# Optimization experiments

Hardware: AMD Instinct MI355X
Metric: run time of the kernel (lower is better)

The kernel has to match this reference:

```python
import jax, jax.numpy as jnp
import numpy as np

N_GENE = 50000
N_PROT = 50000
E = 500000
D = 128          # embedding_dim
C = 32           # out_channels = embedding_dim // attn_heads
F_IN = 256       # in_channels per node type
NUM_MP = 3       # metapaths: [gene-gene, gene-protein, protein-protein]


def _glorot(key, shape):
    lim = float(np.sqrt(6.0 / (shape[0] + shape[1])))
    return jax.random.uniform(key, shape, minval=-lim, maxval=lim, dtype=jnp.float32)


def setup_inputs() -> dict:
    key = jax.random.key(0)
    ks = jax.random.split(key, 24)
    inp = {
        "x_gene": jax.random.normal(ks[0], (N_GENE, F_IN), dtype=jnp.float32),
        "x_protein": jax.random.normal(ks[1], (N_PROT, F_IN), dtype=jnp.float32),
        # node-type projections linear_l / linear_r
        "Wl_gene": _glorot(ks[2], (D, F_IN)), "bl_gene": jnp.zeros((D,), jnp.float32),
        "Wr_gene": _glorot(ks[3], (D, F_IN)), "br_gene": jnp.zeros((D,), jnp.float32),
        "Wl_prot": _glorot(ks[4], (D, F_IN)), "bl_prot": jnp.zeros((D,), jnp.float32),
        "Wr_prot": _glorot(ks[5], (D, F_IN)), "br_prot": jnp.zeros((D,), jnp.float32),
        # per-metapath attention params (stacked over 3 metapaths)
        "alW": jnp.stack([_glorot(ks[6 + i], (C, D)) for i in range(NUM_MP)]),
        "alb": jnp.zeros((NUM_MP, C), jnp.float32),
        "arW": jnp.stack([_glorot(ks[9 + i], (C, D)) for i in range(NUM_MP)]),
        "arb": jnp.zeros((NUM_MP, C), jnp.float32),
        "qw": jnp.stack([_glorot(ks[12 + i], (2 * C, 1)) for i in range(NUM_MP)]),
        "sharp": jnp.ones((NUM_MP,), jnp.float32),  # 'sharpening' alpha_activation
        # per-node-type relation-weighting conv (Linear(D, 1))
        "conv_gene_W": _glorot(ks[15], (1, D)), "conv_gene_b": jnp.zeros((1,), jnp.float32),
        "conv_prot_W": _glorot(ks[16], (1, D)), "conv_prot_b": jnp.zeros((1,), jnp.float32),
        # edge indices: row 0 = head node (aggregation target), row 1 = tail node
        "edge_gg": jax.random.randint(ks[17], (2, E), 0, N_GENE, dtype=jnp.int32),
        "edge_gp": jnp.stack([jax.random.randint(ks[18], (E,), 0, N_GENE, dtype=jnp.int32),
                               jax.random.randint(ks[19], (E,), 0, N_PROT, dtype=jnp.int32)]),
        "edge_pp": jax.random.randint(ks[20], (2, E), 0, N_PROT, dtype=jnp.int32),
    }
    return inp


def _segment_softmax(scores, seg, n):
    # numerically stable softmax over variable-size neighborhoods (grouped by seg)
    m = jax.ops.segment_max(scores, seg, num_segments=n)
    m = jnp.where(jnp.isfinite(m), m, 0.0)
    ex = jnp.exp(scores - m[seg])
    denom = jax.ops.segment_sum(ex, seg, num_segments=n)
    return ex / (denom[seg] + 1e-16)


def _metapath_agg(l_head, r_tail, alW, alb, arW, arb, qw, sharp, eidx, n_head):
    # alpha_l / alpha_r node-level projections [N, C]
    al = l_head @ alW.T + alb
    ar = r_tail @ arW.T + arb
    src, dst = eidx[0], eidx[1]           # head (aggregate-at), tail (message-from)
    a_i = al[src]                          # [E, C]
    a_j = ar[dst]                          # [E, C]
    # attn_q: Tanh then Linear(2C -> 1, no bias); 'sharpening' scales the logit
    e = (jnp.tanh(jnp.concatenate([a_i, a_j], axis=1)) @ qw)[:, 0] * sharp  # [E]
    alpha = _segment_softmax(e, src, n_head)
    # message x_j * alpha, scatter-add into head nodes (aggr='add')
    return jax.ops.segment_sum(r_tail[dst] * alpha[:, None], src, num_segments=n_head)


def _relation_combine(aggs, l_self, conv_W, conv_b):
    # stack relation embeddings + self embedding: [N, R, D]
    out = jnp.stack(aggs + [l_self], axis=1)
    beta = jax.nn.softmax(out @ conv_W.T + conv_b, axis=1)  # [N, R, 1]
    return jax.nn.relu(jnp.sum(out * beta, axis=1))          # [N, D]


def reference(x_gene, x_protein, Wl_gene, bl_gene, Wr_gene, br_gene,
              Wl_prot, bl_prot, Wr_prot, br_prot,
              alW, alb, arW, arb, qw, sharp,
              conv_gene_W, conv_gene_b, conv_prot_W, conv_prot_b,
              edge_gg, edge_gp, edge_pp):
    # first layer: l/r projections from raw features
    l_gene = x_gene @ Wl_gene.T + bl_gene
    r_gene = x_gene @ Wr_gene.T + br_gene
    l_prot = x_protein @ Wl_prot.T + bl_prot
    r_prot = x_protein @ Wr_prot.T + br_prot

    # metapath 0: gene <- gene ; metapath 1: gene <- protein ; metapath 2: protein <- protein
    agg_gg = _metapath_agg(l_gene, r_gene, alW[0], alb[0], arW[0], arb[0], qw[0], sharp[0], edge_gg, N_GENE)
    agg_gp = _metapath_agg(l_gene, r_prot, alW[1], alb[1], arW[1], arb[1], qw[1], sharp[1], edge_gp, N_GENE)
    agg_pp = _metapath_agg(l_prot, r_prot, alW[2], alb[2], arW[2], arb[2], qw[2], sharp[2], edge_pp, N_PROT)

    out_gene = _relation_combine([agg_gg, agg_gp], l_gene, conv_gene_W, conv_gene_b)
    out_prot = _relation_combine([agg_pp], l_prot, conv_prot_W, conv_prot_b)
    return (out_gene, out_prot)
```

## Files before the change

### kernel.cpp

```cpp
#include <hip/hip_runtime.h>
#include <hip/hip_bf16.h>


typedef __attribute__((ext_vector_type(8))) short short8;
typedef __attribute__((ext_vector_type(4))) float floatx4;

__device__ __forceinline__ void gload16(const void* g, void* l) {
  __builtin_amdgcn_global_load_lds(
      (const __attribute__((address_space(1))) void*)g,
      (__attribute__((address_space(3))) void*)l, 16, 0, 0);
}

__device__ __forceinline__ ushort f2b(float x) {
  __hip_bfloat16 h = __float2bfloat16(x);
  return *reinterpret_cast<ushort*>(&h);
}
__device__ __forceinline__ float b2f_lo(unsigned v) { return __uint_as_float(v << 16); }
__device__ __forceinline__ float b2f_hi(unsigned v) { return __uint_as_float(v & 0xffff0000u); }

struct CvtArgs {
  const float* src[8];
  ushort* dst[8];
  int valid[8];
  int total[8];
  int bstart[9];
};
__global__ __launch_bounds__(256) void cvt_multi(CvtArgs a) {
  int b = blockIdx.x;
  int e = 0;
#pragma unroll
  for (int j = 1; j < 8; ++j)
    if (b >= a.bstart[j]) e = j;
  int i = ((b - a.bstart[e]) * 256 + threadIdx.x) * 4;
  if (i >= a.total[e]) return;
  float4 v = make_float4(0.f, 0.f, 0.f, 0.f);
  if (i < a.valid[e]) v = *(const float4*)(a.src[e] + i);
  ushort4 o;
  o.x = f2b(v.x); o.y = f2b(v.y); o.z = f2b(v.z); o.w = f2b(v.w);
  *(ushort4*)(a.dst[e] + i) = o;
}

struct ProjArgs {
  const float* x[2];
  const ushort* Wb[2];
  const float* bl[2];
  const float* br[2];
  ushort* lb[2];
  ushort* rb[2];
  int N[2];
  const ushort* aW[4];
  const float* ab[4];
  const float* q0[4];
  const float* q1[4];
  float* o0[4];
  float* o1[4];
  int BN[4];
};
__global__ __launch_bounds__(256) void proj_lr_mfma(ProjArgs g) {
  const int ty = blockIdx.z;
  const float* xp = g.x[ty];
  const int N = g.N[ty];
  __shared__ float Asf[2 * 128 * 32];
  __shared__ ushort Bs[2 * 128 * 32];
  const int tid = threadIdx.x;
  const int lane = tid & 63;
  const int wv = tid >> 6;
  const int wm = wv & 1, wn = wv >> 1;
  const int rowBase = blockIdx.x * 128;
  const int colHalf = blockIdx.y;
  const ushort* Wbase = g.Wb[ty] + (size_t)colHalf * 128 * 256;

  floatx4 acc[4][4] = {};

  auto stage = [&](int buf, int k0) {
#pragma unroll
    for (int i = 0; i < 4; ++i) {
      const int G = i * 256 + wv * 64 + lane;
      const int row = G >> 3;
      const int cg = (G & 7) ^ (row & 7);
      const int xr = min(rowBase + row, N - 1);
      gload16(xp + (size_t)xr * 256 + k0 + cg * 4, &Asf[buf * 4096 + G * 4]);
    }
#pragma unroll
    for (int i = 0; i < 2; ++i) {
      const int G = i * 256 + wv * 64 + lane;
      const int row = G >> 2;
      const int cg = (G & 3) ^ ((row >> 1) & 3);
      gload16(Wbase + (size_t)row * 256 + k0 + cg * 8, &Bs[buf * 4096 + G * 8]);
    }
  };

  stage(0, 0);
  __syncthreads();

  int t = 0;
  for (int k0 = 0; k0 < 256; k0 += 32) {
    if (k0 < 224) stage(t ^ 1, k0 + 32);
    const float* Ab = &Asf[t * 4096];
    const ushort* Bb = &Bs[t * 4096];
    short8 bf[4];
#pragma unroll
    for (int nt = 0; nt < 4; ++nt) {
      const int row = wn * 64 + nt * 16 + (lane & 15);
      const int c = (lane >> 4) ^ ((row >> 1) & 3);
      bf[nt] = *(const short8*)&Bb[(row * 4 + c) * 8];
    }
#pragma unroll
    for (int mt = 0; mt < 4; ++mt) {
      const int row = wm * 64 + mt * 16 + (lane & 15);
      const int c0 = ((lane >> 4) * 2) ^ (row & 7);
      const int c1 = ((lane >> 4) * 2 + 1) ^ (row & 7);
      float4 f0 = *(const float4*)&Ab[(row * 8 + c0) * 4];
      float4 f1 = *(const float4*)&Ab[(row * 8 + c1) * 4];
      short8 a;
      a[0] = (short)f2b(f0.x); a[1] = (short)f2b(f0.y);
      a[2] = (short)f2b(f0.z); a[3] = (short)f2b(f0.w);
      a[4] = (short)f2b(f1.x); a[5] = (short)f2b(f1.y);
      a[6] = (short)f2b(f1.z); a[7] = (short)f2b(f1.w);
#pragma unroll
      for (int nt = 0; nt < 4; ++nt)
        acc[mt][nt] = __builtin_amdgcn_mfma_f32_16x16x32_bf16(a, bf[nt], acc[mt][nt], 0, 0, 0);
    }
    __syncthreads();
    t ^= 1;
  }

  ushort* tile = (ushort*)Asf;
  const float* bias = colHalf ? g.br[ty] : g.bl[ty];
  ushort* outp = colHalf ? g.rb[ty] : g.lb[ty];
#pragma unroll
  for (int mt = 0; mt < 4; ++mt)
#pragma unroll
    for (int nt = 0; nt < 4; ++nt) {
      int col = wn * 64 + nt * 16 + (lane & 15);
      float bv = bias[col];
#pragma unroll
      for (int vi = 0; vi < 4; ++vi) {
        int row = wm * 64 + mt * 16 + (lane >> 4) * 4 + vi;
        ushort v = f2b(acc[mt][nt][vi] + bv);
        tile[row * 128 + (((col >> 3) ^ (row & 15)) << 3) + (col & 7)] = v;
        if (rowBase + row < N) outp[(size_t)(rowBase + row) * 128 + col] = v;
      }
    }
  __syncthreads();

  const int e = ty * 2 + colHalf;
  const int NB = g.BN[e] >> 4;
  const ushort* aW = g.aW[e];
  floatx4 acc2[2][4] = {};
  for (int k0 = 0; k0 < 128; k0 += 32) {
    short8 bf2[4];
#pragma unroll
    for (int nt = 0; nt < 4; ++nt)
      if (nt < NB)
        bf2[nt] = *(const short8*)(aW + (size_t)(nt * 16 + (lane & 15)) * 128 +
                                   k0 + (lane >> 4) * 8);
#pragma unroll
    for (int mt = 0; mt < 2; ++mt) {
      const int row = wv * 32 + mt * 16 + (lane & 15);
      const int c8 = (k0 >> 3) + (lane >> 4);
      short8 a = *(const short8*)&tile[row * 128 + ((c8 ^ (row & 15)) << 3)];
#pragma unroll
      for (int nt = 0; nt < 4; ++nt)
        if (nt < NB)
          acc2[mt][nt] = __builtin_amdgcn_mfma_f32_16x16x32_bf16(a, bf2[nt], acc2[mt][nt], 0, 0, 0);
    }
  }

  const float* ab = g.ab[e];
  const int l15 = lane & 15;
  const bool two = (NB == 4);
  float bv2[4];
#pragma unroll
  for (int nt = 0; nt < 4; ++nt) bv2[nt] = (nt < NB) ? ab[nt * 16 + l15] : 0.f;
  float q0v0 = g.q0[e][l15], q0v1 = g.q0[e][16 + l15];
  float q1v0 = 0.f, q1v1 = 0.f;
  if (two) { q1v0 = g.q1[e][l15]; q1v1 = g.q1[e][16 + l15]; }
  float* o0 = g.o0[e];
  float* o1 = g.o1[e];
#pragma unroll
  for (int mt = 0; mt < 2; ++mt)
#pragma unroll
    for (int vi = 0; vi < 4; ++vi) {
      float slo = tanhf(acc2[mt][0][vi] + bv2[0]) * q0v0
                + tanhf(acc2[mt][1][vi] + bv2[1]) * q0v1;
      float shi = 0.f;
      if (two)
        shi = tanhf(acc2[mt][2][vi] + bv2[2]) * q1v0
            + tanhf(acc2[mt][3][vi] + bv2[3]) * q1v1;
#pragma unroll
      for (int m = 8; m >= 1; m >>= 1) {
        slo += __shfl_xor(slo, m, 64);
        shi += __shfl_xor(shi, m, 64);
      }
      const int row = rowBase + wv * 32 + mt * 16 + (lane >> 4) * 4 + vi;
      if (l15 == 0 && row < N) {
        o0[row] = slo;
        if (two) o1[row] = shi;
      }
    }
}

__global__ __launch_bounds__(256) void hist3_kernel(
    const int* __restrict__ e0, const int* __restrict__ e1,
    const int* __restrict__ e2, int* __restrict__ deg,
    int* __restrict__ rank, int E, int NG) {
  int e = blockIdx.x * 256 + threadIdx.x;
  if (e >= 3 * E) return;
  int mp = (e >= 2 * E) ? 2 : ((e >= E) ? 1 : 0);
  int el = e - mp * E;
  const int* ep = (mp == 0) ? e0 : (mp == 1) ? e1 : e2;
  int segb = (mp == 2) ? 2 * NG : mp * NG;
  rank[e] = atomicAdd(&deg[segb + ep[el]], 1);
}

__global__ __launch_bounds__(256) void scanA_kernel(
    const int* __restrict__ deg, int* __restrict__ offsets,
    int* __restrict__ tile_tot, int n) {
  __shared__ int wtot[4];
  const int t = threadIdx.x;
  const int base = blockIdx.x * 2048 + t * 8;
  int v[8], pre[8], s = 0;
#pragma unroll
  for (int j = 0; j < 8; ++j) {
    v[j] = (base + j < n) ? deg[base + j] : 0;
    pre[j] = s;
    s += v[j];
  }
  const int lane = t & 63, wv = t >> 6;
  int x = s;
#pragma unroll
  for (int o = 1; o < 64; o <<= 1) {
    int u = __shfl_up(x, o, 64);
    if (lane >= o) x += u;
  }
  if (lane == 63) wtot[wv] = x;
  __syncthreads();
  int wpre = 0;
#pragma unroll
  for (int j = 0; j < 4; ++j) wpre += (j < wv) ? wtot[j] : 0;
  int excl = wpre + x - s;
#pragma unroll
  for (int j = 0; j < 8; ++j)
    if (base + j < n) offsets[base + j] = excl + pre[j];
  if (t == 255) tile_tot[blockIdx.x] = wpre + x;
}

__global__ __launch_bounds__(256) void scanB_kernel(
    const int* __restrict__ tile_tot, int* __restrict__ tile_pre,
    int* __restrict__ offsets, int T, int n) {
  __shared__ int wtot[4];
  const int t = threadIdx.x;
  int v = (t < T) ? tile_tot[t] : 0;
  const int lane = t & 63, wv = t >> 6;
  int x = v;
#pragma unroll
  for (int o = 1; o < 64; o <<= 1) {
    int u = __shfl_up(x, o, 64);
    if (lane >= o) x += u;
  }
  if (lane == 63) wtot[wv] = x;
  __syncthreads();
  int wpre = 0;
#pragma unroll
  for (int j = 0; j < 4; ++j) wpre += (j < wv) ? wtot[j] : 0;
  if (t < T) tile_pre[t] = wpre + x - v;
  if (t == 255) offsets[n] = wpre + x;
}

__global__ __launch_bounds__(256) void scanC_kernel(
    int* __restrict__ offsets, const int* __restrict__ tile_pre, int n) {
  const int add = tile_pre[blockIdx.x];
  const int base = blockIdx.x * 2048 + threadIdx.x * 8;
#pragma unroll
  for (int j = 0; j < 8; ++j)
    if (base + j < n) offsets[base + j] += add;
}

__global__ __launch_bounds__(256) void scatter3_kernel(
    const int* __restrict__ e0, const int* __restrict__ e1,
    const int* __restrict__ e2, const int* __restrict__ rank,
    const int* __restrict__ offsets,
    const float* __restrict__ tl3, const float* __restrict__ tr3,
    const float* __restrict__ sharp, int2* __restrict__ recs,
    int E, int NG, int NP) {
  int e = blockIdx.x * 256 + threadIdx.x;
  if (e >= 3 * E) return;
  int mp = (e >= 2 * E) ? 2 : ((e >= E) ? 1 : 0);
  int el = e - mp * E;
  const int* ep = (mp == 0) ? e0 : (mp == 1) ? e1 : e2;
  int s = ep[el], d = ep[el + E];
  int hb = (mp == 2) ? 2 * NG : mp * NG;
  int tb = (mp == 0) ? 0 : (mp == 1) ? NG : NG + NP;
  float w = expf((tl3[hb + s] + tr3[tb + d]) * sharp[mp]);
  recs[offsets[hb + s] + rank[e]] = make_int2(d << 8, __float_as_int(w));
}

__global__ __launch_bounds__(256) void gather_combine(
    const ushort* __restrict__ rb_gene, const ushort* __restrict__ rb_prot,
    const ushort* __restrict__ lb_gene, const ushort* __restrict__ lb_prot,
    const int* __restrict__ offsets, const int2* __restrict__ recs,
    const float* __restrict__ cgW, const float* __restrict__ cgb,
    const float* __restrict__ cpW, const float* __restrict__ cpb,
    float* __restrict__ out_gene, float* __restrict__ out_prot,
    int NG, int NP) {
  const int lane = threadIdx.x & 63;
  const int l16 = lane & 15;
  const int node = blockIdx.x * 16 + (threadIdx.x >> 4);
  if (node >= NG + NP) return;
  const bool isGene = node < NG;
  const unsigned coloff = (unsigned)l16 << 4;
  const unsigned OMASK = 0x00FFFF00u;

  const int h0 = isGene ? node : NG + node;
  const int j0a = offsets[h0];
  const int ca = offsets[h0 + 1] - j0a;
  int j0b = 0, cb2 = 0;
  if (isGene) {
    j0b = offsets[NG + node];
    cb2 = offsets[NG + node + 1] - j0b;
  }

  float a0[8] = {0.f, 0.f, 0.f, 0.f, 0.f, 0.f, 0.f, 0.f};
  float a1[8] = {0.f, 0.f, 0.f, 0.f, 0.f, 0.f, 0.f, 0.f};
  float ds0 = 0.f, ds1 = 0.f;
  const ushort* rtA = isGene ? rb_gene : rb_prot;

  if (isGene) {
    const int cmax = (ca > cb2) ? ca : cb2;
    if (cmax > 0) {
      int2 rA[4], rB[4];
#pragma unroll
      for (int p = 0; p < 4; ++p) {
        rA[p] = recs[j0a + ((p < ca) ? p : 0)];
        rB[p] = recs[j0b + ((p < cb2) ? p : 0)];
      }
      const int nit = (cmax + 3) >> 2;
      for (int it = 0; it < nit; ++it) {
        const int b = it * 4;
        float wA[4], wB[4];
        uint4 vA[4], vB[4];
#pragma unroll
        for (int p = 0; p < 4; ++p) {
          wA[p] = (b + p < ca)  ? __int_as_float(rA[p].y) : 0.f;
          wB[p] = (b + p < cb2) ? __int_as_float(rB[p].y) : 0.f;
          vA[p] = *(const uint4*)((const char*)rtA + (((unsigned)rA[p].x & OMASK) + coloff));
          vB[p] = *(const uint4*)((const char*)rb_prot + (((unsigned)rB[p].x & OMASK) + coloff));
        }
        const int nb = b + 4;
#pragma unroll
        for (int p = 0; p < 4; ++p) {
          rA[p] = recs[j0a + ((nb + p < ca) ? nb + p : 0)];
          rB[p] = recs[j0b + ((nb + p < cb2) ? nb + p : 0)];
        }
#pragma unroll
        for (int p = 0; p < 4; ++p) {
          ds0 += wA[p];
          a0[0] += b2f_lo(vA[p].x) * wA[p]; a0[1] += b2f_hi(vA[p].x) * wA[p];
          a0[2] += b2f_lo(vA[p].y) * wA[p]; a0[3] += b2f_hi(vA[p].y) * wA[p];
          a0[4] += b2f_lo(vA[p].z) * wA[p]; a0[5] += b2f_hi(vA[p].z) * wA[p];
          a0[6] += b2f_lo(vA[p].w) * wA[p]; a0[7] += b2f_hi(vA[p].w) * wA[p];
          ds1 += wB[p];
          a1[0] += b2f_lo(vB[p].x) * wB[p]; a1[1] += b2f_hi(vB[p].x) * wB[p];
          a1[2] += b2f_lo(vB[p].y) * wB[p]; a1[3] += b2f_hi(vB[p].y) * wB[p];
          a1[4] += b2f_lo(vB[p].z) * wB[p]; a1[5] += b2f_hi(vB[p].z) * wB[p];
          a1[6] += b2f_lo(vB[p].w) * wB[p]; a1[7] += b2f_hi(vB[p].w) * wB[p];
        }
      }
    }
  } else {
    if (ca > 0) {
      int2 r0 = recs[j0a];
      int2 r1 = recs[j0a + ((1 < ca) ? 1 : 0)];
      int2 r2 = recs[j0a + ((2 < ca) ? 2 : 0)];
      int2 r3 = recs[j0a + ((3 < ca) ? 3 : 0)];
      const int nit = (ca + 3) >> 2;
      for (int it = 0; it < nit; ++it) {
        const int b = it * 4;
        const float w0 = (b < ca)     ? __int_as_float(r0.y) : 0.f;
        const float w1 = (b + 1 < ca) ? __int_as_float(r1.y) : 0.f;
        const float w2 = (b + 2 < ca) ? __int_as_float(r2.y) : 0.f;
        const float w3 = (b + 3 < ca) ? __int_as_float(r3.y) : 0.f;
        const uint4 v0 = *(const uint4*)((const char*)rtA + (((unsigned)r0.x & OMASK) + coloff));
        const uint4 v1 = *(const uint4*)((const char*)rtA + (((unsigned)r1.x & OMASK) + coloff));
        const uint4 v2 = *(const uint4*)((const char*)rtA + (((unsigned)r2.x & OMASK) + coloff));
        const uint4 v3 = *(const uint4*)((const char*)rtA + (((unsigned)r3.x & OMASK) + coloff));
        const int nb = b + 4;
        r0 = recs[j0a + ((nb < ca) ? nb : 0)];
        r1 = recs[j0a + ((nb + 1 < ca) ? nb + 1 : 0)];
        r2 = recs[j0a + ((nb + 2 < ca) ? nb + 2 : 0)];
        r3 = recs[j0a + ((nb + 3 < ca) ? nb + 3 : 0)];
        ds0 += (w0 + w1) + (w2 + w3);
        a0[0] += b2f_lo(v0.x) * w0 + b2f_lo(v1.x) * w1 + b2f_lo(v2.x) * w2 + b2f_lo(v3.x) * w3;
        a0[1] += b2f_hi(v0.x) * w0 + b2f_hi(v1.x) * w1 + b2f_hi(v2.x) * w2 + b2f_hi(v3.x) * w3;
        a0[2] += b2f_lo(v0.y) * w0 + b2f_lo(v1.y) * w1 + b2f_lo(v2.y) * w2 + b2f_lo(v3.y) * w3;
        a0[3] += b2f_hi(v0.y) * w0 + b2f_hi(v1.y) * w1 + b2f_hi(v2.y) * w2 + b2f_hi(v3.y) * w3;
        a0[4] += b2f_lo(v0.z) * w0 + b2f_lo(v1.z) * w1 + b2f_lo(v2.z) * w2 + b2f_lo(v3.z) * w3;
        a0[5] += b2f_hi(v0.z) * w0 + b2f_hi(v1.z) * w1 + b2f_hi(v2.z) * w2 + b2f_hi(v3.z) * w3;
        a0[6] += b2f_lo(v0.w) * w0 + b2f_lo(v1.w) * w1 + b2f_lo(v2.w) * w2 + b2f_lo(v3.w) * w3;
        a0[7] += b2f_hi(v0.w) * w0 + b2f_hi(v1.w) * w1 + b2f_hi(v2.w) * w2 + b2f_hi(v3.w) * w3;
      }
    }
  }

  const float inv0 = 1.f / (ds0 + 1e-16f);
  const float inv1 = 1.f / (ds1 + 1e-16f);
  float g0[8], g1[8], self[8];
#pragma unroll
  for (int c = 0; c < 8; ++c) { g0[c] = a0[c] * inv0; g1[c] = a1[c] * inv1; }
  {
    const ushort* lbp = isGene ? lb_gene + (size_t)node * 128
                               : lb_prot + (size_t)(node - NG) * 128;
    uint4 sv = *(const uint4*)(lbp + l16 * 8);
    self[0] = b2f_lo(sv.x); self[1] = b2f_hi(sv.x);
    self[2] = b2f_lo(sv.y); self[3] = b2f_hi(sv.y);
    self[4] = b2f_lo(sv.z); self[5] = b2f_hi(sv.z);
    self[6] = b2f_lo(sv.w); self[7] = b2f_hi(sv.w);
  }

  const float* cW = isGene ? cgW : cpW;
  const float cb = isGene ? cgb[0] : cpb[0];
  const float4 wlo = *(const float4*)(cW + l16 * 8);
  const float4 whi = *(const float4*)(cW + l16 * 8 + 4);
  float p0 = g0[0] * wlo.x + g0[1] * wlo.y + g0[2] * wlo.z + g0[3] * wlo.w +
             g0[4] * whi.x + g0[5] * whi.y + g0[6] * whi.z + g0[7] * whi.w;
  float p1 = g1[0] * wlo.x + g1[1] * wlo.y + g1[2] * wlo.z + g1[3] * wlo.w +
             g1[4] * whi.x + g1[5] * whi.y + g1[6] * whi.z + g1[7] * whi.w;
  float ps = self[0] * wlo.x + self[1] * wlo.y + self[2] * wlo.z + self[3] * wlo.w +
             self[4] * whi.x + self[5] * whi.y + self[6] * whi.z + self[7] * whi.w;
#pragma unroll
  for (int m = 8; m >= 1; m >>= 1) {
    p0 += __shfl_xor(p0, m, 64);
    p1 += __shfl_xor(p1, m, 64);
    ps += __shfl_xor(ps, m, 64);
  }
  const float s0 = p0 + cb, s1 = p1 + cb, ss = ps + cb;
  const float mx = isGene ? fmaxf(fmaxf(s0, s1), ss) : fmaxf(s0, ss);
  const float e0 = expf(s0 - mx);
  const float e1 = isGene ? expf(s1 - mx) : 0.f;
  const float es = expf(ss - mx);
  const float sum = e0 + e1 + es;
  const float b0 = e0 / sum, b1 = e1 / sum, bs = es / sum;

  float4 o0, o1;
  o0.x = fmaxf(g0[0] * b0 + g1[0] * b1 + self[0] * bs, 0.f);
  o0.y = fmaxf(g0[1] * b0 + g1[1] * b1 + self[1] * bs, 0.f);
  o0.z = fmaxf(g0[2] * b0 + g1[2] * b1 + self[2] * bs, 0.f);
  o0.w = fmaxf(g0[3] * b0 + g1[3] * b1 + self[3] * bs, 0.f);
  o1.x = fmaxf(g0[4] * b0 + g1[4] * b1 + self[4] * bs, 0.f);
  o1.y = fmaxf(g0[5] * b0 + g1[5] * b1 + self[5] * bs, 0.f);
  o1.z = fmaxf(g0[6] * b0 + g1[6] * b1 + self[6] * bs, 0.f);
  o1.w = fmaxf(g0[7] * b0 + g1[7] * b1 + self[7] * bs, 0.f);
  float* op = isGene ? out_gene + (size_t)node * 128
                     : out_prot + (size_t)(node - NG) * 128;
  *(float4*)(op + l16 * 8) = o0;
  *(float4*)(op + l16 * 8 + 4) = o1;
}

extern "C" void kernel_launch(void* const* d_in, const int* in_sizes, int n_in,
                              void* d_out, int out_size, void* d_ws,
                              size_t ws_size, hipStream_t stream) {
  const float* x_gene  = (const float*)d_in[0];
  const float* x_prot  = (const float*)d_in[1];
  const float* Wl_gene = (const float*)d_in[2];
  const float* bl_gene = (const float*)d_in[3];
  const float* Wr_gene = (const float*)d_in[4];
  const float* br_gene = (const float*)d_in[5];
  const float* Wl_prot = (const float*)d_in[6];
  const float* bl_prot = (const float*)d_in[7];
  const float* Wr_prot = (const float*)d_in[8];
  const float* br_prot = (const float*)d_in[9];
  const float* alW     = (const float*)d_in[10];
  const float* alb     = (const float*)d_in[11];
  const float* arW     = (const float*)d_in[12];
  const float* arb     = (const float*)d_in[13];
  const float* qw      = (const float*)d_in[14];
  const float* sharp   = (const float*)d_in[15];
  const float* cgW     = (const float*)d_in[16];
  const float* cgb     = (const float*)d_in[17];
  const float* cpW     = (const float*)d_in[18];
  const float* cpb     = (const float*)d_in[19];
  const int* e_gg      = (const int*)d_in[20];
  const int* e_gp      = (const int*)d_in[21];
  const int* e_pp      = (const int*)d_in[22];

  const int NG = in_sizes[0] / 256;
  const int NP = in_sizes[1] / 256;
  const int E  = in_sizes[20] / 2;
  const int NPG = (NG + 127) & ~127;
  const int NT = 2 * NG + NP;
  const int NR = NG + 2 * NP;

  char* base = (char*)d_ws;
  size_t off = 0;
  auto alloc = [&](size_t bytes) {
    void* p = base + off;
    off = (off + bytes + 255) & ~(size_t)255;
    return p;
  };
  ushort* Wlr_gene = (ushort*)alloc(256 * 256 * 2);
  ushort* Wlr_prot = (ushort*)alloc(256 * 256 * 2);
  ushort* alWb     = (ushort*)alloc(96 * 128 * 2);
  ushort* arWb     = (ushort*)alloc(96 * 128 * 2);
  ushort* lb_gene  = (ushort*)alloc((size_t)NPG * 128 * 2);
  ushort* rb_gene  = (ushort*)alloc((size_t)NPG * 128 * 2);
  ushort* lb_prot  = (ushort*)alloc((size_t)NPG * 128 * 2);
  ushort* rb_prot  = (ushort*)alloc((size_t)NPG * 128 * 2);
  int*    deg      = (int*)alloc((size_t)NT * 4);
  int*    offsets  = (int*)alloc((size_t)(NT + 1) * 4);
  const int TILES  = (NT + 2047) / 2048;
  int*    tile_tot = (int*)alloc((size_t)TILES * 4);
  int*    tile_pre = (int*)alloc((size_t)TILES * 4);
  int*    rank     = (int*)alloc((size_t)(3 * E) * 4);
  int2*   recs     = (int2*)alloc((size_t)(3 * E) * sizeof(int2));
  float*  tl3      = (float*)alloc((size_t)NT * 4);
  float*  tr3      = (float*)alloc((size_t)NR * 4);

  float* out_gene = (float*)d_out;
  float* out_prot = out_gene + (size_t)NG * 128;

  dim3 blk(256);

  {
    CvtArgs a;
    const float* srcs[8] = {Wl_gene, Wr_gene, Wl_prot, Wr_prot, alW, arW,
                            Wl_gene, Wl_gene};
    ushort* dsts[8] = {Wlr_gene, Wlr_gene + 128 * 256,
                       Wlr_prot, Wlr_prot + 128 * 256, alWb, arWb,
                       Wlr_gene, Wlr_gene};
    int sizes[8] = {128 * 256, 128 * 256, 128 * 256, 128 * 256,
                    96 * 128, 96 * 128, 0, 0};
    int b = 0;
    for (int j = 0; j < 8; ++j) {
      a.src[j] = srcs[j]; a.dst[j] = dsts[j];
      a.valid[j] = sizes[j]; a.total[j] = sizes[j];
      a.bstart[j] = b;
      b += (sizes[j] / 4 + 255) / 256;
    }
    a.bstart[8] = b;
    cvt_multi<<<b, blk, 0, stream>>>(a);
  }

  {
    ProjArgs p;
    p.x[0] = x_gene; p.x[1] = x_prot;
    p.Wb[0] = Wlr_gene; p.Wb[1] = Wlr_prot;
    p.bl[0] = bl_gene; p.bl[1] = bl_prot;
    p.br[0] = br_gene; p.br[1] = br_prot;
    p.lb[0] = lb_gene; p.lb[1] = lb_prot;
    p.rb[0] = rb_gene; p.rb[1] = rb_prot;
    p.N[0] = NG; p.N[1] = NP;
    p.aW[0] = alWb;            p.ab[0] = alb;      p.BN[0] = 64;
    p.q0[0] = qw + 0;  p.q1[0] = qw + 64;  p.o0[0] = tl3;          p.o1[0] = tl3 + NG;
    p.aW[1] = arWb;            p.ab[1] = arb;      p.BN[1] = 32;
    p.q0[1] = qw + 32; p.q1[1] = qw + 32;  p.o0[1] = tr3;          p.o1[1] = tr3;
    p.aW[2] = alWb + 64 * 128; p.ab[2] = alb + 64; p.BN[2] = 32;
    p.q0[2] = qw + 128; p.q1[2] = qw + 128; p.o0[2] = tl3 + 2 * NG; p.o1[2] = tl3 + 2 * NG;
    p.aW[3] = arWb + 32 * 128; p.ab[3] = arb + 32; p.BN[3] = 64;
    p.q0[3] = qw + 96; p.q1[3] = qw + 160; p.o0[3] = tr3 + NG;     p.o1[3] = tr3 + NG + NP;
    proj_lr_mfma<<<dim3(NPG / 128, 2, 2), blk, 0, stream>>>(p);
  }

  const int gridE3 = (3 * E + 255) / 256;
  hipMemsetAsync(deg, 0, (size_t)NT * sizeof(int), stream);
  hist3_kernel<<<gridE3, blk, 0, stream>>>(e_gg, e_gp, e_pp, deg, rank, E, NG);
  scanA_kernel<<<TILES, blk, 0, stream>>>(deg, offsets, tile_tot, NT);
  scanB_kernel<<<1, blk, 0, stream>>>(tile_tot, tile_pre, offsets, TILES, NT);
  scanC_kernel<<<TILES, blk, 0, stream>>>(offsets, tile_pre, NT);
  scatter3_kernel<<<gridE3, blk, 0, stream>>>(e_gg, e_gp, e_pp, rank, offsets,
                                              tl3, tr3, sharp, recs, E, NG, NP);

  gather_combine<<<(NG + NP + 15) / 16, blk, 0, stream>>>(
      rb_gene, rb_prot, lb_gene, lb_prot, offsets, recs,
      cgW, cgb, cpW, cpb, out_gene, out_prot, NG, NP);
}
```

Measured before the change: 398.1 us.

## Fuse edge histogram into projection kernel launch as extra blocks

Merges the edge-degree histogram (atomic counting with rank capture) into the projection GEMM kernel by appending extra blocks that do the histogram work. The grid is flattened to 1D, with block index decoding for type, column half and row tile. This removes one kernel launch and lets the memory-bound atomic work overlap with the compute-bound MFMA projection. The cost is that the histogram blocks now carry the GEMM kernel's large shared-memory allocation, which may limit how many of them can be resident at once.

```diff
diff --git a/kernel.cpp b/kernel.cpp
--- a/kernel.cpp
+++ b/kernel.cpp
@@ -55,19 +55,42 @@
   float* o0[4];
   float* o1[4];
   int BN[4];
+  const int* e0;
+  const int* e1;
+  const int* e2;
+  int* deg;
+  int* rank;
+  int E;
+  int NGh;
+  int projBlocks;
 };
 __global__ __launch_bounds__(256) void proj_lr_mfma(ProjArgs g) {
-  const int ty = blockIdx.z;
-  const float* xp = g.x[ty];
-  const int N = g.N[ty];
   __shared__ float Asf[2 * 128 * 32];
   __shared__ ushort Bs[2 * 128 * 32];
   const int tid = threadIdx.x;
+
+  if ((int)blockIdx.x >= g.projBlocks) {
+    const int E = g.E;
+    int e = ((int)blockIdx.x - g.projBlocks) * 256 + tid;
+    if (e < 3 * E) {
+      int mp = (e >= 2 * E) ? 2 : ((e >= E) ? 1 : 0);
+      int el = e - mp * E;
+      const int* ep = (mp == 0) ? g.e0 : (mp == 1) ? g.e1 : g.e2;
+      int segb = (mp == 2) ? 2 * g.NGh : mp * g.NGh;
+      g.rank[e] = atomicAdd(&g.deg[segb + ep[el]], 1);
+    }
+    return;
+  }
+
+  const int pb = blockIdx.x;
+  const int ty = pb & 1;
+  const int colHalf = (pb >> 1) & 1;
+  const float* xp = g.x[ty];
+  const int N = g.N[ty];
   const int lane = tid & 63;
   const int wv = tid >> 6;
   const int wm = wv & 1, wn = wv >> 1;
-  const int rowBase = blockIdx.x * 128;
-  const int colHalf = blockIdx.y;
+  const int rowBase = (pb >> 2) * 128;
   const ushort* Wbase = g.Wb[ty] + (size_t)colHalf * 128 * 256;
 
   floatx4 acc[4][4] = {};
@@ -199,19 +222,6 @@
         if (two) o1[row] = shi;
       }
     }
-}
-
-__global__ __launch_bounds__(256) void hist3_kernel(
-    const int* __restrict__ e0, const int* __restrict__ e1,
-    const int* __restrict__ e2, int* __restrict__ deg,
-    int* __restrict__ rank, int E, int NG) {
-  int e = blockIdx.x * 256 + threadIdx.x;
-  if (e >= 3 * E) return;
-  int mp = (e >= 2 * E) ? 2 : ((e >= E) ? 1 : 0);
-  int el = e - mp * E;
-  const int* ep = (mp == 0) ? e0 : (mp == 1) ? e1 : e2;
-  int segb = (mp == 2) ? 2 * NG : mp * NG;
-  rank[e] = atomicAdd(&deg[segb + ep[el]], 1);
 }
 
 __global__ __launch_bounds__(256) void scanA_kernel(
@@ -521,6 +531,7 @@
 
   dim3 blk(256);
 
+  hipMemsetAsync(deg, 0, (size_t)NT * sizeof(int), stream);
   {
     CvtArgs a;
     const float* srcs[8] = {Wl_gene, Wr_gene, Wl_prot, Wr_prot, alW, arW,
@@ -541,6 +552,8 @@
     cvt_multi<<<b, blk, 0, stream>>>(a);
   }
 
+  const int gridE3 = (3 * E + 255) / 256;
+  const int projBlocks = (NPG / 128) * 4;
   {
     ProjArgs p;
     p.x[0] = x_gene; p.x[1] = x_prot;
@@ -558,12 +571,12 @@
     p.q0[2] = qw + 128; p.q1[2] = qw + 128; p.o0[2] = tl3 + 2 * NG; p.o1[2] = tl3 + 2 * NG;
     p.aW[3] = arWb + 32 * 128; p.ab[3] = arb + 32; p.BN[3] = 64;
     p.q0[3] = qw + 96; p.q1[3] = qw + 160; p.o0[3] = tr3 + NG;     p.o1[3] = tr3 + NG + NP;
-    proj_lr_mfma<<<dim3(NPG / 128, 2, 2), blk, 0, stream>>>(p);
-  }
-
-  const int gridE3 = (3 * E + 255) / 256;
-  hipMemsetAsync(deg, 0, (size_t)NT * sizeof(int), stream);
-  hist3_kernel<<<gridE3, blk, 0, stream>>>(e_gg, e_gp, e_pp, deg, rank, E, NG);
+    p.e0 = e_gg; p.e1 = e_gp; p.e2 = e_pp;
+    p.deg = deg; p.rank = rank; p.E = E; p.NGh = NG;
+    p.projBlocks = projBlocks;
+    proj_lr_mfma<<<projBlocks + gridE3, blk, 0, stream>>>(p);
+  }
+
   scanA_kernel<<<TILES, blk, 0, stream>>>(deg, offsets, tile_tot, NT);
   scanB_kernel<<<1, blk, 0, stream>>>(tile_tot, tile_pre, offsets, TILES, NT);
   scanC_kernel<<<TILES, blk, 0, stream>>>(offsets, tile_pre, NT);
```

Result: faster. 384.7 us (-3.4%).
